# Optimization experiments

Hardware: AMD Instinct MI355X
Metric: run time of the kernel (lower is better)

Reference implementation:

```python
import math
import jax, jax.numpy as jnp
import numpy as np

N_HEAD = 12
HEAD_DIM = 64
NEG = -1e9

def setup_inputs() -> dict:
    key = jax.random.key(0)
    k1, k2, k3 = jax.random.split(key, 3)
    B, T, C = 16, 1024, 768
    x = jax.random.normal(k1, (B, T, C), dtype=jnp.float32)
    attention_mask = jnp.ones((B, T), dtype=jnp.int32)
    W_attn = jax.random.normal(k2, (C, 3 * C), dtype=jnp.float32) * 0.02
    b_attn = jnp.zeros((3 * C,), dtype=jnp.float32)
    W_proj = jax.random.normal(k3, (C, C), dtype=jnp.float32) * 0.02
    b_proj = jnp.zeros((C,), dtype=jnp.float32)
    return {"x": x, "attention_mask": attention_mask, "W_attn": W_attn,
            "b_attn": b_attn, "W_proj": W_proj, "b_proj": b_proj}

def reference(x, attention_mask, W_attn, b_attn, W_proj, b_proj):
    B, T, C = x.shape
    H, D = N_HEAD, HEAD_DIM
    qkv = x @ W_attn + b_attn                       # [B,T,3C]
    q, k, v = jnp.split(qkv, 3, axis=-1)
    q = q.reshape(B, T, H, D).transpose(0, 2, 1, 3)  # [B,H,T,D]
    k = k.reshape(B, T, H, D).transpose(0, 2, 1, 3)
    v = v.reshape(B, T, H, D).transpose(0, 2, 1, 3)
    att = jnp.einsum('bhqd,bhkd->bhqk', q, k) / math.sqrt(D)  # [B,H,T,T]
    causal = jnp.tril(jnp.ones((T, T), dtype=bool))[None, None]
    key_mask = (attention_mask[:, None, None, :] != 0)          # [B,1,1,T]
    # masked_fill(-inf) then replace inf with -1e9 == set masked to -1e9
    att = jnp.where(causal & key_mask, att, NEG)
    att = jax.nn.softmax(att, axis=-1)
    query_mask = attention_mask[:, None, :, None].astype(att.dtype)  # [B,1,T,1]
    att = att * query_mask
    y = jnp.einsum('bhqk,bhkd->bhqd', att, v)        # [B,H,T,D]
    y = y.transpose(0, 2, 1, 3).reshape(B, T, C)
    return y @ W_proj + b_proj
```

## Files before the change

### kernel.cpp

```cpp
#include <hip/hip_runtime.h>
#include <stdint.h>

typedef unsigned short u16;
typedef unsigned int u32;
typedef __attribute__((ext_vector_type(8))) short short8;
typedef __attribute__((ext_vector_type(4))) float f32x4;
typedef __attribute__((ext_vector_type(4))) unsigned short u16x4;

#define LDS_AS __attribute__((address_space(3)))
#define GLB_AS __attribute__((address_space(1)))

__device__ __forceinline__ u16 f2bf(float f) {
  u32 u = __float_as_uint(f);
  u = (u + 0x7FFFu + ((u >> 16) & 1u)) >> 16;
  return (u16)u;
}

__device__ __forceinline__ void gload_lds16(const u16* g, u16* l) {
  __builtin_amdgcn_global_load_lds((const GLB_AS u32*)g, (LDS_AS u32*)l, 16, 0, 0);
}

__device__ __forceinline__ f32x4 mfma16(short8 a, short8 b, f32x4 c) {
  return __builtin_amdgcn_mfma_f32_16x16x32_bf16(a, b, c, 0, 0, 0);
}

__global__ __launch_bounds__(256) void k_cvt(const float* __restrict__ in,
                                             u16* __restrict__ out, int n4) {
  int i = blockIdx.x * 256 + threadIdx.x;
  if (i >= n4) return;
  f32x4 v = ((const f32x4*)in)[i];
  u16x4 o = {f2bf(v[0]), f2bf(v[1]), f2bf(v[2]), f2bf(v[3])};
  ((u16x4*)out)[i] = o;
}

__global__ __launch_bounds__(256) void k_transpose_cvt(const float* __restrict__ W,
                                                       u16* __restrict__ Wt, int K, int N) {
  __shared__ float tile[32][33];
  int n0 = blockIdx.x * 32;
  int k0 = blockIdx.y * 32;
  int tx = threadIdx.x & 31, ty = threadIdx.x >> 5;
#pragma unroll
  for (int i = 0; i < 4; i++) {
    int k = k0 + ty + i * 8;
    tile[ty + i * 8][tx] = W[(size_t)k * N + n0 + tx];
  }
  __syncthreads();
#pragma unroll
  for (int i = 0; i < 4; i++) {
    int n = n0 + ty + i * 8;
    Wt[(size_t)n * K + k0 + tx] = f2bf(tile[tx][ty + i * 8]);
  }
}

template <int MODE>
__global__ __launch_bounds__(256) void k_gemm(const u16* __restrict__ A,
                                              const u16* __restrict__ Bt,
                                              const float* __restrict__ bias,
                                              void* __restrict__ C, u16* __restrict__ vTo,
                                              int M, int N, int K) {
  __shared__ __align__(16) u16 As[2][128 * 64];
  __shared__ __align__(16) u16 Bs[2][128 * 64];
  const int nwg = gridDim.x;
  const int wgo = blockIdx.x;
  const int cpx = nwg >> 3;
  const int swz = (wgo & 7) * cpx + (wgo >> 3);
  const int ntn = N >> 7;
  const int tm = swz / ntn, tn = swz % ntn;
  const int m0 = tm << 7, n0 = tn << 7;
  const int tid = threadIdx.x;
  const int lane = tid & 63, w = tid >> 6;
  const int wm = (w >> 1) << 6, wn = (w & 1) << 6;
  const int fr = lane & 15, kg = lane >> 4;

  f32x4 acc[4][4];
#pragma unroll
  for (int i = 0; i < 4; i++)
#pragma unroll
    for (int j = 0; j < 4; j++) acc[i][j] = (f32x4){0.f, 0.f, 0.f, 0.f};

  const int rs = tid >> 3;
  const int ck = (((tid & 7) ^ (rs & 7)) << 3);
  const u16* ga = A + (size_t)(m0 + rs) * K + ck;
  const u16* gb = Bt + (size_t)(n0 + rs) * K + ck;
  const size_t row32 = (size_t)32 * K;

#define GSTAGE(buf, kt)                                                      \
  {                                                                          \
    const int ko = (kt) * 64;                                                \
    _Pragma("unroll") for (int s = 0; s < 4; ++s) {                          \
      gload_lds16(ga + s * row32 + ko, &As[buf][s * 2048 + tid * 8]);        \
    }                                                                        \
    _Pragma("unroll") for (int s = 0; s < 4; ++s) {                          \
      gload_lds16(gb + s * row32 + ko, &Bs[buf][s * 2048 + tid * 8]);        \
    }                                                                        \
  }

  const int KT = K >> 6;
  GSTAGE(0, 0);

  for (int kt = 0; kt < KT; ++kt) {
    const int cur = kt & 1;
    if (kt + 1 < KT) {
      GSTAGE(cur ^ 1, kt + 1);
      asm volatile("s_waitcnt vmcnt(8)" ::: "memory");
    } else {
      asm volatile("s_waitcnt vmcnt(0)" ::: "memory");
    }
    __builtin_amdgcn_sched_barrier(0);
    __builtin_amdgcn_s_barrier();
    __builtin_amdgcn_sched_barrier(0);

#pragma unroll
    for (int kk = 0; kk < 2; ++kk) {
      short8 af[4], bf[4];
      const int cs = ((kk * 4 + kg) ^ (fr & 7)) << 3;
#pragma unroll
      for (int mi = 0; mi < 4; mi++)
        af[mi] = *(const short8*)&As[cur][(wm + mi * 16 + fr) * 64 + cs];
#pragma unroll
      for (int nj = 0; nj < 4; nj++)
        bf[nj] = *(const short8*)&Bs[cur][(wn + nj * 16 + fr) * 64 + cs];
      asm volatile("s_waitcnt lgkmcnt(0)" ::: "memory");
      __builtin_amdgcn_sched_barrier(0);
#pragma unroll
      for (int mi = 0; mi < 4; mi++)
#pragma unroll
        for (int nj = 0; nj < 4; nj++)
          acc[mi][nj] = mfma16(af[mi], bf[nj], acc[mi][nj]);
    }
    __builtin_amdgcn_sched_barrier(0);
    __builtin_amdgcn_s_barrier();
  }
#undef GSTAGE

  const int r0 = (lane >> 4) << 2;
  const bool isv = (MODE == 1) && (n0 >= 1536);
#pragma unroll
  for (int mi = 0; mi < 4; mi++) {
    const int row = m0 + wm + mi * 16 + r0;
#pragma unroll
    for (int nj = 0; nj < 4; nj++) {
      const int col = n0 + wn + nj * 16 + fr;
      const float bs = bias[col];
      f32x4 v = acc[mi][nj];
      if (MODE == 0) {
#pragma unroll
        for (int r = 0; r < 4; r++)
          ((float*)C)[(size_t)(row + r) * N + col] = v[r] + bs;
      } else if (!isv) {
#pragma unroll
        for (int r = 0; r < 4; r++)
          ((u16*)C)[(size_t)(row + r) * 1536 + col] = f2bf(v[r] + bs);
      } else {
        int d = col - 1536;
        int hh = d >> 6, dd = d & 63;
        int bb = row >> 10, t = row & 1023;
        u16x4 pk = {f2bf(v[0] + bs), f2bf(v[1] + bs), f2bf(v[2] + bs), f2bf(v[3] + bs)};
        *(u16x4*)&vTo[((size_t)(bb * 12 + hh) * 64 + dd) * 1024 + t] = pk;
      }
    }
  }
}

__global__ __launch_bounds__(256, 3) void k_attn(const u16* __restrict__ qk,
                                                 const u16* __restrict__ vT,
                                                 const int* __restrict__ amask,
                                                 u16* __restrict__ y) {
  __shared__ __align__(16) u16 Ks[2][64 * 64];
  __shared__ __align__(16) u16 Vs[2][64 * 64];
  __shared__ __align__(16) u16 Ps[4][2][16 * 72];

  const int bh = blockIdx.x;
  const int qp = blockIdx.y;
  const int b = bh / 12, h = bh % 12;
  const int qbA = qp * 64, qbB = (15 - qp) * 64;
  const int nt = 16 - qp;
  const int tid = threadIdx.x, lane = tid & 63, w = tid >> 6;
  const int fr = lane & 15, kg = lane >> 4;

  const u16* qg = qk + (size_t)b * 1024 * 1536 + h * 64;
  const u16* kgp = qg + 768;
  const u16* vg = vT + (size_t)bh * 64 * 1024;
  const int* mrow = amask + b * 1024;

  short8 qfA[2], qfB[2];
  {
    const u16* ra = qg + (size_t)(qbA + w * 16 + fr) * 1536 + kg * 8;
    const u16* rb = qg + (size_t)(qbB + w * 16 + fr) * 1536 + kg * 8;
    qfA[0] = *(const short8*)ra;
    qfA[1] = *(const short8*)(ra + 32);
    qfB[0] = *(const short8*)rb;
    qfB[1] = *(const short8*)(rb + 32);
  }

  const int sr0 = tid >> 3, sc = tid & 7;
  const int sr1 = sr0 + 32;
  const int sw0 = (sc ^ (sr0 & 7)) << 3;

#define STAGE_KV(buf, kv0)                                                          \
  {                                                                                 \
    gload_lds16(kgp + (size_t)((kv0) + sr0) * 1536 + sw0, &Ks[buf][tid * 8]);       \
    gload_lds16(kgp + (size_t)((kv0) + sr1) * 1536 + sw0, &Ks[buf][2048 + tid * 8]);\
    gload_lds16(vg + (size_t)sr0 * 1024 + (kv0) + sw0, &Vs[buf][tid * 8]);          \
    gload_lds16(vg + (size_t)sr1 * 1024 + (kv0) + sw0, &Vs[buf][2048 + tid * 8]);   \
  }

  STAGE_KV(0, 0);

  f32x4 oA[4], oB[4];
  float mA[4], lA[4], mB[4], lB[4];
#pragma unroll
  for (int i = 0; i < 4; i++) {
    oA[i] = (f32x4){0.f, 0.f, 0.f, 0.f};
    oB[i] = (f32x4){0.f, 0.f, 0.f, 0.f};
    mA[i] = -1e30f; lA[i] = 0.f;
    mB[i] = -1e30f; lB[i] = 0.f;
  }
  u16* PwA = &Ps[w][0][0];
  u16* PwB = &Ps[w][1][0];

  __syncthreads();

  for (int it = 0; it < nt; ++it) {
    const int kv0 = it * 64;
    const int cur = it & 1;
    if (it + 1 < nt) STAGE_KV(cur ^ 1, kv0 + 64);
    const bool aAct = (it <= qp);
    const u16* Kc = Ks[cur];
    const u16* Vc = Vs[cur];

    f32x4 sA[4], sB[4];
#pragma unroll
    for (int nf = 0; nf < 4; nf++) {
      sA[nf] = (f32x4){0.f, 0.f, 0.f, 0.f};
      sB[nf] = (f32x4){0.f, 0.f, 0.f, 0.f};
    }
#pragma unroll
    for (int nf = 0; nf < 4; nf++) {
      const int base = (nf * 16 + fr) * 64;
      short8 k0 = *(const short8*)&Kc[base + ((kg ^ (fr & 7)) << 3)];
      short8 k1 = *(const short8*)&Kc[base + (((kg + 4) ^ (fr & 7)) << 3)];
      sB[nf] = mfma16(qfB[0], k0, sB[nf]);
      sB[nf] = mfma16(qfB[1], k1, sB[nf]);
      if (aAct) {
        sA[nf] = mfma16(qfA[0], k0, sA[nf]);
        sA[nf] = mfma16(qfA[1], k1, sA[nf]);
      }
    }

    float kmok[4];
#pragma unroll
    for (int nf = 0; nf < 4; nf++)
      kmok[nf] = (mrow[kv0 + nf * 16 + fr] != 0) ? 0.f : -1e9f;

    auto softmax = [&](f32x4(&s)[4], float(&mr)[4], float(&lr)[4], f32x4(&oa)[4],
                       u16* Pw, int qb, bool diag) {
#pragma unroll
      for (int nf = 0; nf < 4; nf++)
#pragma unroll
        for (int r = 0; r < 4; r++) {
          float v = s[nf][r] * 0.125f + kmok[nf];
          if (diag) {
            int kv = kv0 + nf * 16 + fr;
            int q = qb + w * 16 + kg * 4 + r;
            if (kv > q) v = -1e9f;
          }
          s[nf][r] = v;
        }
      float mnw[4];
#pragma unroll
      for (int r = 0; r < 4; r++) {
        float m = fmaxf(fmaxf(s[0][r], s[1][r]), fmaxf(s[2][r], s[3][r]));
        m = fmaxf(m, __shfl_xor(m, 1));
        m = fmaxf(m, __shfl_xor(m, 2));
        m = fmaxf(m, __shfl_xor(m, 4));
        m = fmaxf(m, __shfl_xor(m, 8));
        float mnew = fmaxf(mr[r], m);
        float alpha = __expf(mr[r] - mnew);
        mr[r] = mnew;
        mnw[r] = mnew;
        lr[r] *= alpha;
        oa[0][r] *= alpha; oa[1][r] *= alpha;
        oa[2][r] *= alpha; oa[3][r] *= alpha;
      }
      float psum[4] = {0.f, 0.f, 0.f, 0.f};
#pragma unroll
      for (int nf = 0; nf < 4; nf++)
#pragma unroll
        for (int r = 0; r < 4; r++) {
          float e = __expf(s[nf][r] - mnw[r]);
          psum[r] += e;
          Pw[(kg * 4 + r) * 72 + nf * 16 + fr] = f2bf(e);
        }
#pragma unroll
      for (int r = 0; r < 4; r++) {
        float ssum = psum[r];
        ssum += __shfl_xor(ssum, 1);
        ssum += __shfl_xor(ssum, 2);
        ssum += __shfl_xor(ssum, 4);
        ssum += __shfl_xor(ssum, 8);
        lr[r] += ssum;
      }
    };

    if (aAct) softmax(sA, mA, lA, oA, PwA, qbA, it == qp);
    softmax(sB, mB, lB, oB, PwB, qbB, it == nt - 1);

#pragma unroll
    for (int kc = 0; kc < 2; kc++) {
      short8 pB = *(const short8*)&PwB[fr * 72 + kc * 32 + kg * 8];
      short8 pA;
      if (aAct) pA = *(const short8*)&PwA[fr * 72 + kc * 32 + kg * 8];
#pragma unroll
      for (int df = 0; df < 4; df++) {
        short8 vf = *(const short8*)&Vc[(df * 16 + fr) * 64 + (((kc * 4 + kg) ^ (fr & 7)) << 3)];
        oB[df] = mfma16(pB, vf, oB[df]);
        if (aAct) oA[df] = mfma16(pA, vf, oA[df]);
      }
    }
    __syncthreads();
  }

#pragma unroll
  for (int r = 0; r < 4; r++) {
    int qA = qbA + w * 16 + kg * 4 + r;
    int qB = qbB + w * 16 + kg * 4 + r;
    float nA = (mrow[qA] != 0) ? (1.f / lA[r]) : 0.f;
    float nB = (mrow[qB] != 0) ? (1.f / lB[r]) : 0.f;
#pragma unroll
    for (int df = 0; df < 4; df++) {
      y[(size_t)(b * 1024 + qA) * 768 + h * 64 + df * 16 + fr] = f2bf(oA[df][r] * nA);
      y[(size_t)(b * 1024 + qB) * 768 + h * 64 + df * 16 + fr] = f2bf(oB[df][r] * nB);
    }
  }
}

extern "C" void kernel_launch(void* const* d_in, const int* in_sizes, int n_in,
                              void* d_out, int out_size, void* d_ws, size_t ws_size,
                              hipStream_t stream) {
  const float* x = (const float*)d_in[0];
  const int* amask = (const int*)d_in[1];
  const float* W_attn = (const float*)d_in[2];
  const float* b_attn = (const float*)d_in[3];
  const float* W_proj = (const float*)d_in[4];
  const float* b_proj = (const float*)d_in[5];
  float* out = (float*)d_out;

  u16* xb = (u16*)d_ws;
  u16* wta = xb + (size_t)16384 * 768;
  u16* wtp = wta + (size_t)2304 * 768;
  u16* qk = wtp + (size_t)768 * 768;
  u16* vT = qk + (size_t)16384 * 1536;
  u16* yb = vT + (size_t)192 * 64 * 1024;

  (void)in_sizes; (void)n_in; (void)out_size; (void)ws_size;

  k_cvt<<<(16384 * 768 / 4) / 256, 256, 0, stream>>>(x, xb, 16384 * 768 / 4);
  k_transpose_cvt<<<dim3(2304 / 32, 768 / 32), 256, 0, stream>>>(W_attn, wta, 768, 2304);
  k_transpose_cvt<<<dim3(768 / 32, 768 / 32), 256, 0, stream>>>(W_proj, wtp, 768, 768);

  k_gemm<1><<<(16384 / 128) * (2304 / 128), 256, 0, stream>>>(xb, wta, b_attn, qk, vT,
                                                              16384, 2304, 768);
  k_attn<<<dim3(192, 8), 256, 0, stream>>>(qk, vT, amask, yb);
  k_gemm<0><<<(16384 / 128) * (768 / 128), 256, 0, stream>>>(yb, wtp, b_proj, out, nullptr,
                                                             16384, 768, 768);
}
```

Baseline: 236.1 us.

## Pipeline attention loop with explicit waitcnt barriers, bitmask mask, exp2 softmax, priorities

Reworks the attention inner loop synchronization. It replaces __syncthreads with explicit vmcnt waits so that only the current KV tile's async loads are awaited while the next tile's prefetch stays in flight. It also precomputes the key mask as LDS bitmasks via ballot instead of reading global memory every iteration, folds log2e into the scale so exp2f replaces __expf, and raises wave priority around the MFMA blocks. This reduces sync stalls and per-iteration global loads, but it depends on hand-counted vmcnt values that must match the number of outstanding loads.

```diff
diff --git a/kernel.cpp b/kernel.cpp
--- a/kernel.cpp
+++ b/kernel.cpp
@@ -169,6 +169,7 @@
   __shared__ __align__(16) u16 Ks[2][64 * 64];
   __shared__ __align__(16) u16 Vs[2][64 * 64];
   __shared__ __align__(16) u16 Ps[4][2][16 * 72];
+  __shared__ u32 mbits[32];
 
   const int bh = blockIdx.x;
   const int qp = blockIdx.y;
@@ -193,6 +194,18 @@
     qfB[1] = *(const short8*)(rb + 32);
   }
 
+#pragma unroll
+  for (int i = 0; i < 4; i++) {
+    int tok = i * 256 + tid;
+    unsigned long long bm = __ballot(mrow[tok] != 0);
+    if (lane == 0) {
+      int base = (i * 256 + w * 64) >> 5;
+      mbits[base] = (u32)bm;
+      mbits[base + 1] = (u32)(bm >> 32);
+    }
+  }
+  __syncthreads();
+
   const int sr0 = tid >> 3, sc = tid & 7;
   const int sr1 = sr0 + 32;
   const int sw0 = (sc ^ (sr0 & 7)) << 3;
@@ -219,12 +232,21 @@
   u16* PwA = &Ps[w][0][0];
   u16* PwB = &Ps[w][1][0];
 
-  __syncthreads();
+  const float SCALE2 = 0.125f * 1.44269504f;
 
   for (int it = 0; it < nt; ++it) {
     const int kv0 = it * 64;
     const int cur = it & 1;
-    if (it + 1 < nt) STAGE_KV(cur ^ 1, kv0 + 64);
+    if (it + 1 < nt) {
+      STAGE_KV(cur ^ 1, kv0 + 64);
+      asm volatile("s_waitcnt vmcnt(4)" ::: "memory");
+    } else {
+      asm volatile("s_waitcnt vmcnt(0)" ::: "memory");
+    }
+    __builtin_amdgcn_sched_barrier(0);
+    __builtin_amdgcn_s_barrier();
+    __builtin_amdgcn_sched_barrier(0);
+
     const bool aAct = (it <= qp);
     const u16* Kc = Ks[cur];
     const u16* Vc = Vs[cur];
@@ -235,6 +257,7 @@
       sA[nf] = (f32x4){0.f, 0.f, 0.f, 0.f};
       sB[nf] = (f32x4){0.f, 0.f, 0.f, 0.f};
     }
+    __builtin_amdgcn_s_setprio(1);
 #pragma unroll
     for (int nf = 0; nf < 4; nf++) {
       const int base = (nf * 16 + fr) * 64;
@@ -247,11 +270,15 @@
         sA[nf] = mfma16(qfA[1], k1, sA[nf]);
       }
     }
+    __builtin_amdgcn_s_setprio(0);
 
     float kmok[4];
 #pragma unroll
-    for (int nf = 0; nf < 4; nf++)
-      kmok[nf] = (mrow[kv0 + nf * 16 + fr] != 0) ? 0.f : -1e9f;
+    for (int nf = 0; nf < 4; nf++) {
+      int kv = kv0 + nf * 16 + fr;
+      u32 wv = mbits[kv >> 5];
+      kmok[nf] = ((wv >> (kv & 31)) & 1u) ? 0.f : -1e9f;
+    }
 
     auto softmax = [&](f32x4(&s)[4], float(&mr)[4], float(&lr)[4], f32x4(&oa)[4],
                        u16* Pw, int qb, bool diag) {
@@ -259,7 +286,7 @@
       for (int nf = 0; nf < 4; nf++)
 #pragma unroll
         for (int r = 0; r < 4; r++) {
-          float v = s[nf][r] * 0.125f + kmok[nf];
+          float v = fmaf(s[nf][r], SCALE2, kmok[nf]);
           if (diag) {
             int kv = kv0 + nf * 16 + fr;
             int q = qb + w * 16 + kg * 4 + r;
@@ -276,7 +303,7 @@
         m = fmaxf(m, __shfl_xor(m, 4));
         m = fmaxf(m, __shfl_xor(m, 8));
         float mnew = fmaxf(mr[r], m);
-        float alpha = __expf(mr[r] - mnew);
+        float alpha = exp2f(mr[r] - mnew);
         mr[r] = mnew;
         mnw[r] = mnew;
         lr[r] *= alpha;
@@ -288,7 +315,7 @@
       for (int nf = 0; nf < 4; nf++)
 #pragma unroll
         for (int r = 0; r < 4; r++) {
-          float e = __expf(s[nf][r] - mnw[r]);
+          float e = exp2f(s[nf][r] - mnw[r]);
           psum[r] += e;
           Pw[(kg * 4 + r) * 72 + nf * 16 + fr] = f2bf(e);
         }
@@ -306,6 +333,7 @@
     if (aAct) softmax(sA, mA, lA, oA, PwA, qbA, it == qp);
     softmax(sB, mB, lB, oB, PwB, qbB, it == nt - 1);
 
+    __builtin_amdgcn_s_setprio(1);
 #pragma unroll
     for (int kc = 0; kc < 2; kc++) {
       short8 pB = *(const short8*)&PwB[fr * 72 + kc * 32 + kg * 8];
@@ -318,8 +346,12 @@
         if (aAct) oA[df] = mfma16(pA, vf, oA[df]);
       }
     }
-    __syncthreads();
-  }
+    __builtin_amdgcn_s_setprio(0);
+
+    __builtin_amdgcn_sched_barrier(0);
+    __builtin_amdgcn_s_barrier();
+  }
+#undef STAGE_KV
 
 #pragma unroll
   for (int r = 0; r < 4; r++) {
```

Result: slower. 258.7 us (+9.6%).
